# Optimization experiments

Hardware: AMD Instinct MI355X
Metric: run time of the kernel (lower is better)

## Reference

```python
import jax, jax.numpy as jnp
import numpy as np

N = 100000
E = 1600000
IN_C = 64
HID = 64
HEADS = 8
HEAD_D = HID // HEADS  # 8
LAYERS = 12
OUT_C = 10
STEPS = 5
NEG_SLOPE = 0.2


def setup_inputs() -> dict:
    key = jax.random.key(0)
    ks = jax.random.split(key, 12)
    x = jax.random.normal(ks[0], (N, IN_C), dtype=jnp.float32)
    edge_index = jax.random.randint(ks[1], (2, E), 0, N, dtype=jnp.int64)
    s = 0.1
    return {
        "x": x,
        "edge_index": edge_index,
        # GAT params: HEADS independent single-head GATConv(in -> HEAD_D)
        "gat_W": jax.random.normal(ks[2], (HEADS, IN_C, HEAD_D), dtype=jnp.float32) * s,
        "gat_a_src": jax.random.normal(ks[3], (HEADS, HEAD_D), dtype=jnp.float32) * s,
        "gat_a_dst": jax.random.normal(ks[4], (HEADS, HEAD_D), dtype=jnp.float32) * s,
        "gat_b": jax.random.normal(ks[5], (HEADS, HEAD_D), dtype=jnp.float32) * s,
        # GCN params: LAYERS x GCNConv(HID -> HID)
        "gcn_W": jax.random.normal(ks[6], (LAYERS, HID, HID), dtype=jnp.float32) * s,
        "gcn_b": jax.random.normal(ks[7], (LAYERS, HID), dtype=jnp.float32) * s,
        # final linear
        "fc_W": jax.random.normal(ks[8], (HID, OUT_C), dtype=jnp.float32) * s,
        "fc_b": jax.random.normal(ks[9], (OUT_C,), dtype=jnp.float32) * s,
    }


def _random_walk(x, row, col):
    # sparse A (COO: row=edge_index[0], col=edge_index[1], vals=1) applied num_steps times
    for _ in range(STEPS):
        x = jax.ops.segment_sum(x[col], row, num_segments=N)
    return x


def _gat_all_heads(x, W, a_src, a_dst, b, src, dst):
    # add self loops
    loop = jnp.arange(N, dtype=src.dtype)
    s2 = jnp.concatenate([src, loop])
    d2 = jnp.concatenate([dst, loop])
    h = jnp.einsum('nf,hfd->nhd', x, W)                      # [N,H,D]
    al_s = jnp.einsum('nhd,hd->nh', h, a_src)                # [N,H]
    al_d = jnp.einsum('nhd,hd->nh', h, a_dst)
    e = jax.nn.leaky_relu(al_s[s2] + al_d[d2], NEG_SLOPE)    # [E+N,H]
    m = jax.ops.segment_max(e, d2, num_segments=N)           # per-target max (self loops -> every node has >=1 edge)
    p = jnp.exp(e - m[d2])
    denom = jax.ops.segment_sum(p, d2, num_segments=N)
    alpha = p / denom[d2]                                    # [E+N,H]
    out = jax.ops.segment_sum(alpha[:, :, None] * h[s2], d2, num_segments=N)  # [N,H,D]
    out = out + b[None, :, :]
    return out.reshape(N, HEADS * HEAD_D)                    # concat heads -> [N,HID]


def _gcn(x, W, b, src, dst):
    loop = jnp.arange(N, dtype=src.dtype)
    s2 = jnp.concatenate([src, loop])
    d2 = jnp.concatenate([dst, loop])
    deg = jax.ops.segment_sum(jnp.ones(s2.shape[0], x.dtype), d2, num_segments=N)
    dis = jnp.where(deg > 0, jax.lax.rsqrt(jnp.maximum(deg, 1.0)), 0.0)
    norm = dis[s2] * dis[d2]                                 # [E+N]
    h = x @ W                                                # [N,HID]
    out = jax.ops.segment_sum(norm[:, None] * h[s2], d2, num_segments=N)
    return out + b


def reference(x, edge_index, gat_W, gat_a_src, gat_a_dst, gat_b, gcn_W, gcn_b, fc_W, fc_b):
    row, col = edge_index[0], edge_index[1]
    # 1) random walk diffusion
    x = _random_walk(x, row, col)
    # 2) multi-head GAT (8 independent heads, concatenated)
    x = _gat_all_heads(x, gat_W, gat_a_src, gat_a_dst, gat_b, row, col)
    # 3) deep residual GCN (faithful to the original indexing quirks)
    initial_residual = x
    for i in range(LAYERS):
        x = _gcn(x, gcn_W[i], gcn_b[i], row, col)
        if i > 0:
            x = x + initial_residual
            initial_residual = x
        x = jax.nn.relu(x)
        if i < LAYERS - 1:
            # note: i-1 == -1 at i==0 -> last layer, as in the torch code
            x = x + _gcn(x, gcn_W[i - 1], gcn_b[i - 1], row, col)
    # 4) final linear
    return x @ fc_W + fc_b
```

## Files before the change

kernel.cpp:

```cpp
#include <hip/hip_runtime.h>


typedef unsigned int u32;

#define BSH 7
#define RNGB 128
#define GEB 256

__device__ __forceinline__ float lrelu(float v) { return v > 0.f ? v : 0.2f * v; }
__device__ __forceinline__ float bf_lo(u32 w) { return __uint_as_float(w << 16); }
__device__ __forceinline__ float bf_hi(u32 w) { return __uint_as_float(w & 0xffff0000u); }
__device__ __forceinline__ u32 pack_bf16(float a, float b) {
  u32 ua = __float_as_uint(a); ua = ua + 0x7fffu + ((ua >> 16) & 1u);
  u32 ub = __float_as_uint(b); ub = ub + 0x7fffu + ((ub >> 16) & 1u);
  return (ua >> 16) | (ub & 0xffff0000u);
}
__device__ __forceinline__ void acc8(float* acc, uint4 q) {
  acc[0] += bf_lo(q.x); acc[1] += bf_hi(q.x);
  acc[2] += bf_lo(q.y); acc[3] += bf_hi(q.y);
  acc[4] += bf_lo(q.z); acc[5] += bf_hi(q.z);
  acc[6] += bf_lo(q.w); acc[7] += bf_hi(q.w);
}
__device__ __forceinline__ void fma8(float* acc, float p, uint4 q) {
  acc[0] = fmaf(p, bf_lo(q.x), acc[0]); acc[1] = fmaf(p, bf_hi(q.x), acc[1]);
  acc[2] = fmaf(p, bf_lo(q.y), acc[2]); acc[3] = fmaf(p, bf_hi(q.y), acc[3]);
  acc[4] = fmaf(p, bf_lo(q.z), acc[4]); acc[5] = fmaf(p, bf_hi(q.z), acc[5]);
  acc[6] = fmaf(p, bf_lo(q.w), acc[6]); acc[7] = fmaf(p, bf_hi(q.w), acc[7]);
}


__global__ __launch_bounds__(256) void k_hist(
    const int* __restrict__ ei, int E, int NB, int chunk,
    int* __restrict__ gHistA, int* __restrict__ gHistB) {
  __shared__ int hA[1024], hB[1024];
  for (int i = threadIdx.x; i < NB; i += 256) { hA[i] = 0; hB[i] = 0; }
  __syncthreads();
  int e0 = blockIdx.x * chunk;
  int e1 = min(E, e0 + chunk);
  for (int e = e0 + threadIdx.x; e < e1; e += 256) {
    int s = ei[e], d = ei[E + e];
    atomicAdd(&hA[s >> BSH], 1);
    atomicAdd(&hB[d >> BSH], 1);
  }
  __syncthreads();
  for (int i = threadIdx.x; i < NB; i += 256) {
    gHistA[blockIdx.x * NB + i] = hA[i];
    gHistB[blockIdx.x * NB + i] = hB[i];
  }
}

__global__ __launch_bounds__(256) void k_colscan(
    int* __restrict__ gHist, int* __restrict__ tot, int NB) {
  __shared__ int s[GEB];
  int b = blockIdx.x;
  int t = threadIdx.x;
  int v = gHist[t * NB + b];
  s[t] = v;
  __syncthreads();
  for (int d = 1; d < GEB; d <<= 1) {
    int u = (t >= d) ? s[t - d] : 0;
    __syncthreads();
    s[t] += u;
    __syncthreads();
  }
  gHist[t * NB + b] = s[t] - v;
  if (t == GEB - 1) tot[b] = s[t];
}

__global__ __launch_bounds__(1024) void k_bscan(
    const int* __restrict__ totA, const int* __restrict__ totB,
    int* __restrict__ baseA, int* __restrict__ baseB,
    int* __restrict__ offA, int* __restrict__ offB, int NB, int N, int E) {
  __shared__ int sa[1024], sb[1024];
  int t = threadIdx.x;
  int va = (t < NB) ? totA[t] : 0;
  int vb = (t < NB) ? totB[t] : 0;
  sa[t] = va; sb[t] = vb;
  __syncthreads();
  for (int d = 1; d < 1024; d <<= 1) {
    int ua = (t >= d) ? sa[t - d] : 0;
    int ub = (t >= d) ? sb[t - d] : 0;
    __syncthreads();
    sa[t] += ua; sb[t] += ub;
    __syncthreads();
  }
  if (t < NB) { baseA[t] = sa[t] - va; baseB[t] = sb[t] - vb; }
  if (t == 0) { offA[N] = E; offB[N] = E; }
}

__global__ __launch_bounds__(256) void k_scatter(
    const int* __restrict__ ei, int E, int NB, int chunk,
    const int* __restrict__ gHistA, const int* __restrict__ gHistB,
    const int* __restrict__ baseA, const int* __restrict__ baseB,
    int2* __restrict__ pairsA, int2* __restrict__ pairsB) {
  __shared__ int cA[1024], cB[1024];
  int g = blockIdx.x;
  for (int i = threadIdx.x; i < NB; i += 256) {
    cA[i] = baseA[i] + gHistA[g * NB + i];
    cB[i] = baseB[i] + gHistB[g * NB + i];
  }
  __syncthreads();
  int e0 = g * chunk;
  int e1 = min(E, e0 + chunk);
  for (int e = e0 + threadIdx.x; e < e1; e += 256) {
    int s = ei[e], d = ei[E + e];
    int pa = atomicAdd(&cA[s >> BSH], 1);
    pairsA[pa] = {s, d};
    int pb = atomicAdd(&cB[d >> BSH], 1);
    pairsB[pb] = {s, d};
  }
}

template <int KEY>
__global__ __launch_bounds__(256) void k_bucket(
    const int2* __restrict__ pairs, const int* __restrict__ base,
    const int* __restrict__ tot, int* __restrict__ off,
    int* __restrict__ idx, float* __restrict__ dis, int N) {
  __shared__ int cnt[RNGB], pfx[RNGB];
  int b = blockIdx.x;
  int node0 = b << BSH;
  int rng = min(RNGB, N - node0);
  int bstart = base[b], bcount = tot[b];
  for (int i = threadIdx.x; i < rng; i += 256) cnt[i] = 0;
  __syncthreads();
  for (int i = threadIdx.x; i < bcount; i += 256) {
    int2 p = pairs[bstart + i];
    int loc = (KEY == 0 ? p.x : p.y) - node0;
    atomicAdd(&cnt[loc], 1);
  }
  __syncthreads();
  if (threadIdx.x == 0) {
    int run = 0;
    for (int i = 0; i < rng; ++i) { pfx[i] = run; run += cnt[i]; }
  }
  __syncthreads();
  for (int i = threadIdx.x; i < rng; i += 256) {
    off[node0 + i] = bstart + pfx[i];
    if (KEY == 1) dis[node0 + i] = rsqrtf((float)(cnt[i] + 1));
  }
  __syncthreads();
  for (int i = threadIdx.x; i < bcount; i += 256) {
    int2 p = pairs[bstart + i];
    int loc = (KEY == 0 ? p.x : p.y) - node0;
    int pos = bstart + atomicAdd(&pfx[loc], 1);
    idx[pos] = (KEY == 0 ? p.y : p.x);
  }
}


template <int FIRST>
__global__ __launch_bounds__(256) void k_rw(
    const int* __restrict__ off, const int* __restrict__ idx,
    const float* __restrict__ Hf, const u32* __restrict__ Hb,
    u32* __restrict__ Xb, int n) {
  int lane = threadIdx.x & 63;
  int wid = threadIdx.x >> 6;
  int d0 = blockIdx.x * 8 + wid * 2;
  if (d0 >= n) return;
  int d1 = d0 + 1;
  bool has1 = d1 < n;
  int rg = lane >> 3, cg = lane & 7;
  const uint4* H4b = (const uint4*)Hb;
  const float4* H4f = (const float4*)Hf;
  int beg0 = off[d0], end0 = off[d0 + 1];
  int beg1 = has1 ? off[d1] : 0, end1 = has1 ? off[d1 + 1] : 0;
  int cnt0 = end0 - beg0, cnt1 = end1 - beg1;
  int cmax = cnt0 > cnt1 ? cnt0 : cnt1;
  float acc0[8], acc1[8];
#pragma unroll
  for (int i = 0; i < 8; ++i) { acc0[i] = 0.f; acc1[i] = 0.f; }
  for (int base = 0; base < cmax; base += 64) {
    int c0 = cnt0 - base; if (c0 > 64) c0 = 64;
    int c1 = cnt1 - base; if (c1 > 64) c1 = 64;
    int sidx0 = (lane < c0) ? idx[beg0 + base + lane] : -1;
    int sidx1 = (lane < c1) ? idx[beg1 + base + lane] : -1;
    int hi = c0 > c1 ? c0 : c1;
    int nI = (hi + 7) >> 3;
    int j = 0;
    for (; j + 2 <= nI; j += 2) {
      int s00 = __shfl(sidx0, j * 8 + rg, 64);
      int s01 = __shfl(sidx0, j * 8 + 8 + rg, 64);
      int s10 = __shfl(sidx1, j * 8 + rg, 64);
      int s11 = __shfl(sidx1, j * 8 + 8 + rg, 64);
      size_t a00 = (size_t)(s00 >= 0 ? s00 : 0);
      size_t a01 = (size_t)(s01 >= 0 ? s01 : 0);
      size_t a10 = (size_t)(s10 >= 0 ? s10 : 0);
      size_t a11 = (size_t)(s11 >= 0 ? s11 : 0);
      if (FIRST) {
        float4 x00 = H4f[a00 * 16 + cg * 2], y00 = H4f[a00 * 16 + cg * 2 + 1];
        float4 x01 = H4f[a01 * 16 + cg * 2], y01 = H4f[a01 * 16 + cg * 2 + 1];
        float4 x10 = H4f[a10 * 16 + cg * 2], y10 = H4f[a10 * 16 + cg * 2 + 1];
        float4 x11 = H4f[a11 * 16 + cg * 2], y11 = H4f[a11 * 16 + cg * 2 + 1];
        if (s00 < 0) { x00 = {0,0,0,0}; y00 = {0,0,0,0}; }
        if (s01 < 0) { x01 = {0,0,0,0}; y01 = {0,0,0,0}; }
        if (s10 < 0) { x10 = {0,0,0,0}; y10 = {0,0,0,0}; }
        if (s11 < 0) { x11 = {0,0,0,0}; y11 = {0,0,0,0}; }
        acc0[0] += x00.x; acc0[1] += x00.y; acc0[2] += x00.z; acc0[3] += x00.w;
        acc0[4] += y00.x; acc0[5] += y00.y; acc0[6] += y00.z; acc0[7] += y00.w;
        acc0[0] += x01.x; acc0[1] += x01.y; acc0[2] += x01.z; acc0[3] += x01.w;
        acc0[4] += y01.x; acc0[5] += y01.y; acc0[6] += y01.z; acc0[7] += y01.w;
        acc1[0] += x10.x; acc1[1] += x10.y; acc1[2] += x10.z; acc1[3] += x10.w;
        acc1[4] += y10.x; acc1[5] += y10.y; acc1[6] += y10.z; acc1[7] += y10.w;
        acc1[0] += x11.x; acc1[1] += x11.y; acc1[2] += x11.z; acc1[3] += x11.w;
        acc1[4] += y11.x; acc1[5] += y11.y; acc1[6] += y11.z; acc1[7] += y11.w;
      } else {
        uint4 q00 = H4b[a00 * 8 + cg];
        uint4 q01 = H4b[a01 * 8 + cg];
        uint4 q10 = H4b[a10 * 8 + cg];
        uint4 q11 = H4b[a11 * 8 + cg];
        if (s00 < 0) q00 = {0u,0u,0u,0u};
        if (s01 < 0) q01 = {0u,0u,0u,0u};
        if (s10 < 0) q10 = {0u,0u,0u,0u};
        if (s11 < 0) q11 = {0u,0u,0u,0u};
        acc8(acc0, q00);
        acc8(acc0, q01);
        acc8(acc1, q10);
        acc8(acc1, q11);
      }
    }
    if (j < nI) {
      int s00 = __shfl(sidx0, j * 8 + rg, 64);
      int s10 = __shfl(sidx1, j * 8 + rg, 64);
      size_t a00 = (size_t)(s00 >= 0 ? s00 : 0);
      size_t a10 = (size_t)(s10 >= 0 ? s10 : 0);
      if (FIRST) {
        float4 x00 = H4f[a00 * 16 + cg * 2], y00 = H4f[a00 * 16 + cg * 2 + 1];
        float4 x10 = H4f[a10 * 16 + cg * 2], y10 = H4f[a10 * 16 + cg * 2 + 1];
        if (s00 < 0) { x00 = {0,0,0,0}; y00 = {0,0,0,0}; }
        if (s10 < 0) { x10 = {0,0,0,0}; y10 = {0,0,0,0}; }
        acc0[0] += x00.x; acc0[1] += x00.y; acc0[2] += x00.z; acc0[3] += x00.w;
        acc0[4] += y00.x; acc0[5] += y00.y; acc0[6] += y00.z; acc0[7] += y00.w;
        acc1[0] += x10.x; acc1[1] += x10.y; acc1[2] += x10.z; acc1[3] += x10.w;
        acc1[4] += y10.x; acc1[5] += y10.y; acc1[6] += y10.z; acc1[7] += y10.w;
      } else {
        uint4 q00 = H4b[a00 * 8 + cg];
        uint4 q10 = H4b[a10 * 8 + cg];
        if (s00 < 0) q00 = {0u,0u,0u,0u};
        if (s10 < 0) q10 = {0u,0u,0u,0u};
        acc8(acc0, q00);
        acc8(acc1, q10);
      }
    }
  }
#pragma unroll
  for (int m = 8; m < 64; m <<= 1)
#pragma unroll
    for (int i = 0; i < 8; ++i) {
      acc0[i] += __shfl_xor(acc0[i], m, 64);
      acc1[i] += __shfl_xor(acc1[i], m, 64);
    }
  if (rg != 0) return;
  uint4 o0 = {pack_bf16(acc0[0], acc0[1]), pack_bf16(acc0[2], acc0[3]),
              pack_bf16(acc0[4], acc0[5]), pack_bf16(acc0[6], acc0[7])};
  ((uint4*)Xb)[(size_t)d0 * 8 + cg] = o0;
  if (has1) {
    uint4 o1 = {pack_bf16(acc1[0], acc1[1]), pack_bf16(acc1[2], acc1[3]),
                pack_bf16(acc1[4], acc1[5]), pack_bf16(acc1[6], acc1[7])};
    ((uint4*)Xb)[(size_t)d1 * 8 + cg] = o1;
  }
}


__global__ __launch_bounds__(256) void k_gat_gemm(
    const u32* __restrict__ Xb, const float* __restrict__ W,
    const float* __restrict__ asrc, const float* __restrict__ adst,
    u32* __restrict__ Hgb, float* __restrict__ al, int n) {
  __shared__ float Xs[64 * 65];
  int row0 = blockIdx.x * 64;
  for (int t = threadIdx.x; t < 512; t += 256) {
    int r = t >> 3, k8 = t & 7;
    int row = row0 + r;
    uint4 xw = (row < n) ? ((const uint4*)Xb)[(size_t)row * 8 + k8]
                         : uint4{0u, 0u, 0u, 0u};
    float* dst = &Xs[r * 65 + k8 * 8];
    dst[0] = bf_lo(xw.x); dst[1] = bf_hi(xw.x);
    dst[2] = bf_lo(xw.y); dst[3] = bf_hi(xw.y);
    dst[4] = bf_lo(xw.z); dst[5] = bf_hi(xw.z);
    dst[6] = bf_lo(xw.w); dst[7] = bf_hi(xw.w);
  }
  __syncthreads();
  int lane = threadIdx.x & 63;
  int w = __builtin_amdgcn_readfirstlane(threadIdx.x >> 6);
  int c0 = w * 16;
  int row = row0 + lane;
  float acc[16];
#pragma unroll
  for (int c = 0; c < 16; ++c) acc[c] = 0.f;
#pragma unroll 4
  for (int k = 0; k < 64; ++k) {
    float xk = Xs[lane * 65 + k];
#pragma unroll
    for (int c = 0; c < 16; ++c) {
      int gc = c0 + c;
      acc[c] = fmaf(xk, W[(gc >> 3) * 512 + k * 8 + (gc & 7)], acc[c]);
    }
  }
  if (row >= n) return;
  float s1a = 0.f, s2a = 0.f, s1b = 0.f, s2b = 0.f;
#pragma unroll
  for (int cc = 0; cc < 8; ++cc) {
    s1a = fmaf(acc[cc], asrc[c0 + cc], s1a);
    s2a = fmaf(acc[cc], adst[c0 + cc], s2a);
    s1b = fmaf(acc[8 + cc], asrc[c0 + 8 + cc], s1b);
    s2b = fmaf(acc[8 + cc], adst[c0 + 8 + cc], s2b);
  }
  float2* al2 = (float2*)al;
  al2[(size_t)row * 8 + w] = {s1a, s1b};
  al2[(size_t)row * 8 + 4 + w] = {s2a, s2b};
  uint4* H4 = (uint4*)Hgb;
  uint4 o0 = {pack_bf16(acc[0], acc[1]), pack_bf16(acc[2], acc[3]),
              pack_bf16(acc[4], acc[5]), pack_bf16(acc[6], acc[7])};
  uint4 o1 = {pack_bf16(acc[8], acc[9]), pack_bf16(acc[10], acc[11]),
              pack_bf16(acc[12], acc[13]), pack_bf16(acc[14], acc[15])};
  H4[(size_t)row * 8 + w * 2] = o0;
  H4[(size_t)row * 8 + w * 2 + 1] = o1;
}

__global__ __launch_bounds__(256) void k_gat_agg(
    const int* __restrict__ off, const int* __restrict__ idx,
    const u32* __restrict__ Hgb, const float* __restrict__ al,
    const float* __restrict__ bias, const float* __restrict__ dis,
    u32* __restrict__ Tout, float* __restrict__ R, int n) {
  int lane = threadIdx.x & 63;
  int wid = threadIdx.x >> 6;
  int d0 = blockIdx.x * 8 + wid * 2;
  if (d0 >= n) return;
  int d1 = d0 + 1;
  bool has1 = d1 < n;
  int rg = lane >> 3, cg = lane & 7;
  const uint4* H4b = (const uint4*)Hgb;
  float ald0 = al[(size_t)d0 * 16 + 8 + cg];
  float es0 = lrelu(al[(size_t)d0 * 16 + cg] + ald0);
  float ald1 = has1 ? al[(size_t)d1 * 16 + 8 + cg] : 0.f;
  float es1 = has1 ? lrelu(al[(size_t)d1 * 16 + cg] + ald1) : 0.f;
  int beg0 = off[d0], end0 = off[d0 + 1];
  int beg1 = has1 ? off[d1] : 0, end1 = has1 ? off[d1 + 1] : 0;
  int cnt0 = end0 - beg0, cnt1 = end1 - beg1;
  int cmax = cnt0 > cnt1 ? cnt0 : cnt1;
  float m0 = es0, m1 = es1;
  for (int base = 0; base < cmax; base += 64) {
    int c0 = cnt0 - base; if (c0 > 64) c0 = 64;
    int c1 = cnt1 - base; if (c1 > 64) c1 = 64;
    int sidx0 = (lane < c0) ? idx[beg0 + base + lane] : -1;
    int sidx1 = (lane < c1) ? idx[beg1 + base + lane] : -1;
    int hi = c0 > c1 ? c0 : c1;
    int nI = (hi + 7) >> 3;
    int j = 0;
    for (; j + 2 <= nI; j += 2) {
      int s00 = __shfl(sidx0, j * 8 + rg, 64);
      int s01 = __shfl(sidx0, j * 8 + 8 + rg, 64);
      int s10 = __shfl(sidx1, j * 8 + rg, 64);
      int s11 = __shfl(sidx1, j * 8 + 8 + rg, 64);
      float a00 = al[(size_t)(s00 >= 0 ? s00 : 0) * 16 + cg];
      float a01 = al[(size_t)(s01 >= 0 ? s01 : 0) * 16 + cg];
      float a10 = al[(size_t)(s10 >= 0 ? s10 : 0) * 16 + cg];
      float a11 = al[(size_t)(s11 >= 0 ? s11 : 0) * 16 + cg];
      if (s00 >= 0) m0 = fmaxf(m0, lrelu(a00 + ald0));
      if (s01 >= 0) m0 = fmaxf(m0, lrelu(a01 + ald0));
      if (s10 >= 0) m1 = fmaxf(m1, lrelu(a10 + ald1));
      if (s11 >= 0) m1 = fmaxf(m1, lrelu(a11 + ald1));
    }
    if (j < nI) {
      int s00 = __shfl(sidx0, j * 8 + rg, 64);
      int s10 = __shfl(sidx1, j * 8 + rg, 64);
      float a00 = al[(size_t)(s00 >= 0 ? s00 : 0) * 16 + cg];
      float a10 = al[(size_t)(s10 >= 0 ? s10 : 0) * 16 + cg];
      if (s00 >= 0) m0 = fmaxf(m0, lrelu(a00 + ald0));
      if (s10 >= 0) m1 = fmaxf(m1, lrelu(a10 + ald1));
    }
  }
#pragma unroll
  for (int mm = 8; mm < 64; mm <<= 1) {
    m0 = fmaxf(m0, __shfl_xor(m0, mm, 64));
    m1 = fmaxf(m1, __shfl_xor(m1, mm, 64));
  }
  float den0 = 0.f, den1 = 0.f;
  float acc0[8], acc1[8];
#pragma unroll
  for (int i = 0; i < 8; ++i) { acc0[i] = 0.f; acc1[i] = 0.f; }
  for (int base = 0; base < cmax; base += 64) {
    int c0 = cnt0 - base; if (c0 > 64) c0 = 64;
    int c1 = cnt1 - base; if (c1 > 64) c1 = 64;
    int sidx0 = (lane < c0) ? idx[beg0 + base + lane] : -1;
    int sidx1 = (lane < c1) ? idx[beg1 + base + lane] : -1;
    int hi = c0 > c1 ? c0 : c1;
    int nI = (hi + 7) >> 3;
    int j = 0;
    for (; j + 2 <= nI; j += 2) {
      int s00 = __shfl(sidx0, j * 8 + rg, 64);
      int s01 = __shfl(sidx0, j * 8 + 8 + rg, 64);
      int s10 = __shfl(sidx1, j * 8 + rg, 64);
      int s11 = __shfl(sidx1, j * 8 + 8 + rg, 64);
      size_t a00 = (size_t)(s00 >= 0 ? s00 : 0);
      size_t a01 = (size_t)(s01 >= 0 ? s01 : 0);
      size_t a10 = (size_t)(s10 >= 0 ? s10 : 0);
      size_t a11 = (size_t)(s11 >= 0 ? s11 : 0);
      float l00 = al[a00 * 16 + cg];
      float l01 = al[a01 * 16 + cg];
      float l10 = al[a10 * 16 + cg];
      float l11 = al[a11 * 16 + cg];
      uint4 q00 = H4b[a00 * 8 + cg];
      uint4 q01 = H4b[a01 * 8 + cg];
      uint4 q10 = H4b[a10 * 8 + cg];
      uint4 q11 = H4b[a11 * 8 + cg];
      float p00 = (s00 >= 0) ? __expf(lrelu(l00 + ald0) - m0) : 0.f;
      float p01 = (s01 >= 0) ? __expf(lrelu(l01 + ald0) - m0) : 0.f;
      float p10 = (s10 >= 0) ? __expf(lrelu(l10 + ald1) - m1) : 0.f;
      float p11 = (s11 >= 0) ? __expf(lrelu(l11 + ald1) - m1) : 0.f;
      den0 += p00; fma8(acc0, p00, q00);
      den0 += p01; fma8(acc0, p01, q01);
      den1 += p10; fma8(acc1, p10, q10);
      den1 += p11; fma8(acc1, p11, q11);
    }
    if (j < nI) {
      int s00 = __shfl(sidx0, j * 8 + rg, 64);
      int s10 = __shfl(sidx1, j * 8 + rg, 64);
      size_t a00 = (size_t)(s00 >= 0 ? s00 : 0);
      size_t a10 = (size_t)(s10 >= 0 ? s10 : 0);
      float l00 = al[a00 * 16 + cg];
      float l10 = al[a10 * 16 + cg];
      uint4 q00 = H4b[a00 * 8 + cg];
      uint4 q10 = H4b[a10 * 8 + cg];
      float p00 = (s00 >= 0) ? __expf(lrelu(l00 + ald0) - m0) : 0.f;
      float p10 = (s10 >= 0) ? __expf(lrelu(l10 + ald1) - m1) : 0.f;
      den0 += p00; fma8(acc0, p00, q00);
      den1 += p10; fma8(acc1, p10, q10);
    }
  }
#pragma unroll
  for (int mm = 8; mm < 64; mm <<= 1) {
#pragma unroll
    for (int i = 0; i < 8; ++i) {
      acc0[i] += __shfl_xor(acc0[i], mm, 64);
      acc1[i] += __shfl_xor(acc1[i], mm, 64);
    }
    den0 += __shfl_xor(den0, mm, 64);
    den1 += __shfl_xor(den1, mm, 64);
  }
  if (rg != 0) return;
#pragma unroll
  for (int nd = 0; nd < 2; ++nd) {
    if (nd == 1 && !has1) break;
    int d = nd == 0 ? d0 : d1;
    float* acc = nd == 0 ? acc0 : acc1;
    float es = nd == 0 ? es0 : es1;
    float m = nd == 0 ? m0 : m1;
    float den = nd == 0 ? den0 : den1;
    float pself = __expf(es - m);
    uint4 hw = H4b[(size_t)d * 8 + cg];
    float hs[8] = {bf_lo(hw.x), bf_hi(hw.x), bf_lo(hw.y), bf_hi(hw.y),
                   bf_lo(hw.z), bf_hi(hw.z), bf_lo(hw.w), bf_hi(hw.w)};
#pragma unroll
    for (int i = 0; i < 8; ++i) acc[i] = fmaf(pself, hs[i], acc[i]);
    den += pself;
    float inv = 1.f / den;
    float4 b0 = ((const float4*)bias)[cg * 2];
    float4 b1 = ((const float4*)bias)[cg * 2 + 1];
    float bv[8] = {b0.x, b0.y, b0.z, b0.w, b1.x, b1.y, b1.z, b1.w};
    float v[8];
#pragma unroll
    for (int i = 0; i < 8; ++i) v[i] = acc[i] * inv + bv[i];
    size_t o0 = (size_t)d * 16 + cg * 2;
    ((float4*)R)[o0] = {v[0], v[1], v[2], v[3]};
    ((float4*)R)[o0 + 1] = {v[4], v[5], v[6], v[7]};
    float dd = dis[d];
    uint4 tw = {pack_bf16(dd * v[0], dd * v[1]), pack_bf16(dd * v[2], dd * v[3]),
                pack_bf16(dd * v[4], dd * v[5]), pack_bf16(dd * v[6], dd * v[7])};
    ((uint4*)Tout)[(size_t)d * 8 + cg] = tw;
  }
}


enum { CG0 = 0, CGR = 1, CGRL = 2, CGD = 3 };

template <int MODE>
__global__ __launch_bounds__(256) void k_conv(
    const int* __restrict__ off, const int* __restrict__ idx,
    const u32* __restrict__ Tin, u32* __restrict__ Tout,
    const float* __restrict__ dis, const float* __restrict__ W,
    const float* __restrict__ bias, float* __restrict__ R,
    float* __restrict__ X, int n) {
  __shared__ float zs[4][128];
  int lane = threadIdx.x & 63;
  int wid = threadIdx.x >> 6;
  int d0 = blockIdx.x * 8 + wid * 2;
  if (d0 >= n) return;
  int d1 = d0 + 1;
  bool has1 = d1 < n;
  int rg = lane >> 3, cg = lane & 7;
  const uint4* T4 = (const uint4*)Tin;
  int beg0 = off[d0], end0 = off[d0 + 1];
  int beg1 = has1 ? off[d1] : 0, end1 = has1 ? off[d1 + 1] : 0;
  int cnt0 = end0 - beg0, cnt1 = end1 - beg1;
  int cmax = cnt0 > cnt1 ? cnt0 : cnt1;
  float acc0[8], acc1[8];
#pragma unroll
  for (int i = 0; i < 8; ++i) { acc0[i] = 0.f; acc1[i] = 0.f; }
  for (int base = 0; base < cmax; base += 64) {
    int c0 = cnt0 - base; if (c0 > 64) c0 = 64;
    int c1 = cnt1 - base; if (c1 > 64) c1 = 64;
    int sidx0 = (lane < c0) ? idx[beg0 + base + lane] : -1;
    int sidx1 = (lane < c1) ? idx[beg1 + base + lane] : -1;
    int hi = c0 > c1 ? c0 : c1;
    int nI = (hi + 7) >> 3;
    int j = 0;
    for (; j + 2 <= nI; j += 2) {
      int s00 = __shfl(sidx0, j * 8 + rg, 64);
      int s01 = __shfl(sidx0, j * 8 + 8 + rg, 64);
      int s10 = __shfl(sidx1, j * 8 + rg, 64);
      int s11 = __shfl(sidx1, j * 8 + 8 + rg, 64);
      size_t a00 = (size_t)(s00 >= 0 ? s00 : 0);
      size_t a01 = (size_t)(s01 >= 0 ? s01 : 0);
      size_t a10 = (size_t)(s10 >= 0 ? s10 : 0);
      size_t a11 = (size_t)(s11 >= 0 ? s11 : 0);
      uint4 q00 = T4[a00 * 8 + cg];
      uint4 q01 = T4[a01 * 8 + cg];
      uint4 q10 = T4[a10 * 8 + cg];
      uint4 q11 = T4[a11 * 8 + cg];
      if (s00 < 0) q00 = {0u,0u,0u,0u};
      if (s01 < 0) q01 = {0u,0u,0u,0u};
      if (s10 < 0) q10 = {0u,0u,0u,0u};
      if (s11 < 0) q11 = {0u,0u,0u,0u};
      acc8(acc0, q00);
      acc8(acc0, q01);
      acc8(acc1, q10);
      acc8(acc1, q11);
    }
    if (j < nI) {
      int s00 = __shfl(sidx0, j * 8 + rg, 64);
      int s10 = __shfl(sidx1, j * 8 + rg, 64);
      size_t a00 = (size_t)(s00 >= 0 ? s00 : 0);
      size_t a10 = (size_t)(s10 >= 0 ? s10 : 0);
      uint4 q00 = T4[a00 * 8 + cg];
      uint4 q10 = T4[a10 * 8 + cg];
      if (s00 < 0) q00 = {0u,0u,0u,0u};
      if (s10 < 0) q10 = {0u,0u,0u,0u};
      acc8(acc0, q00);
      acc8(acc1, q10);
    }
  }
#pragma unroll
  for (int m = 8; m < 64; m <<= 1)
#pragma unroll
    for (int i = 0; i < 8; ++i) {
      acc0[i] += __shfl_xor(acc0[i], m, 64);
      acc1[i] += __shfl_xor(acc1[i], m, 64);
    }
  float dd0 = dis[d0];
  uint4 ts0 = T4[(size_t)d0 * 8 + cg];
  float z0[8] = {dd0 * (acc0[0] + bf_lo(ts0.x)), dd0 * (acc0[1] + bf_hi(ts0.x)),
                 dd0 * (acc0[2] + bf_lo(ts0.y)), dd0 * (acc0[3] + bf_hi(ts0.y)),
                 dd0 * (acc0[4] + bf_lo(ts0.z)), dd0 * (acc0[5] + bf_hi(ts0.z)),
                 dd0 * (acc0[6] + bf_lo(ts0.w)), dd0 * (acc0[7] + bf_hi(ts0.w))};
  float dd1 = has1 ? dis[d1] : 0.f;
  uint4 ts1 = T4[(size_t)(has1 ? d1 : d0) * 8 + cg];
  float z1[8] = {dd1 * (acc1[0] + bf_lo(ts1.x)), dd1 * (acc1[1] + bf_hi(ts1.x)),
                 dd1 * (acc1[2] + bf_lo(ts1.y)), dd1 * (acc1[3] + bf_hi(ts1.y)),
                 dd1 * (acc1[4] + bf_lo(ts1.z)), dd1 * (acc1[5] + bf_hi(ts1.z)),
                 dd1 * (acc1[6] + bf_lo(ts1.w)), dd1 * (acc1[7] + bf_hi(ts1.w))};
  if (rg == 0) {
    float4* zp = (float4*)&zs[wid][cg * 8];
    zp[0] = {z0[0], z0[1], z0[2], z0[3]};
    zp[1] = {z0[4], z0[5], z0[6], z0[7]};
    float4* zq = (float4*)&zs[wid][64 + cg * 8];
    zq[0] = {z1[0], z1[1], z1[2], z1[3]};
    zq[1] = {z1[4], z1[5], z1[6], z1[7]};
  }
  asm volatile("s_waitcnt lgkmcnt(0)" ::: "memory");
  float outc0 = bias[lane];
  float outc1 = outc0;
  const float4* za = (const float4*)&zs[wid][0];
  const float4* zb = (const float4*)&zs[wid][64];
#pragma unroll 4
  for (int k4 = 0; k4 < 16; ++k4) {
    float4 a = za[k4];
    float4 b = zb[k4];
    int k = k4 * 4;
    float w0 = W[(k + 0) * 64 + lane];
    float w1 = W[(k + 1) * 64 + lane];
    float w2 = W[(k + 2) * 64 + lane];
    float w3 = W[(k + 3) * 64 + lane];
    outc0 = fmaf(a.x, w0, outc0); outc1 = fmaf(b.x, w0, outc1);
    outc0 = fmaf(a.y, w1, outc0); outc1 = fmaf(b.y, w1, outc1);
    outc0 = fmaf(a.z, w2, outc0); outc1 = fmaf(b.z, w2, outc1);
    outc0 = fmaf(a.w, w3, outc0); outc1 = fmaf(b.w, w3, outc1);
  }
#pragma unroll
  for (int nd = 0; nd < 2; ++nd) {
    if (nd == 1 && !has1) break;
    int d = nd == 0 ? d0 : d1;
    float outv = nd == 0 ? outc0 : outc1;
    size_t o = (size_t)d * 64 + lane;
    float res;
    if (MODE == CGD) {
      res = X[o] + outv;
    } else if (MODE == CG0) {
      res = fmaxf(outv, 0.f);
      X[o] = res;
    } else {
      float val = outv + R[o];
      R[o] = val;
      res = fmaxf(val, 0.f);
      X[o] = res;
    }
    if (MODE != CGRL) {
      float t = dis[d] * res;
      float tp = __shfl_xor(t, 1, 64);
      if (!(lane & 1))
        Tout[(size_t)d * 32 + (lane >> 1)] = pack_bf16(t, tp);
    }
  }
}


__global__ __launch_bounds__(256) void k_fc(
    const float* __restrict__ X, const float* __restrict__ W,
    const float* __restrict__ b, float* __restrict__ out, int n) {
  __shared__ float Wl[640];
  __shared__ float bl[10];
  for (int i = threadIdx.x; i < 640; i += 256) Wl[i] = W[i];
  if (threadIdx.x < 10) bl[threadIdx.x] = b[threadIdx.x];
  __syncthreads();
  int r = blockIdx.x * blockDim.x + threadIdx.x;
  if (r >= n) return;
  float acc[10];
#pragma unroll
  for (int c = 0; c < 10; ++c) acc[c] = bl[c];
#pragma unroll
  for (int k = 0; k < 64; ++k) {
    float xv = X[(size_t)r * 64 + k];
#pragma unroll
    for (int c = 0; c < 10; ++c) acc[c] = fmaf(xv, Wl[k * 10 + c], acc[c]);
  }
#pragma unroll
  for (int c = 0; c < 10; ++c) out[(size_t)r * 10 + c] = acc[c];
}


extern "C" void kernel_launch(void* const* d_in, const int* in_sizes, int n_in,
                              void* d_out, int out_size, void* d_ws, size_t ws_size,
                              hipStream_t stream) {
  const float* x_in  = (const float*)d_in[0];
  const int*   ei    = (const int*)d_in[1];
  const float* gatW  = (const float*)d_in[2];
  const float* gatAs = (const float*)d_in[3];
  const float* gatAd = (const float*)d_in[4];
  const float* gatB  = (const float*)d_in[5];
  const float* gcnW  = (const float*)d_in[6];
  const float* gcnB  = (const float*)d_in[7];
  const float* fcW   = (const float*)d_in[8];
  const float* fcB   = (const float*)d_in[9];
  float* out = (float*)d_out;

  const int N = in_sizes[0] / 64;
  const int E = in_sizes[1] / 2;
  const int NB = (N + RNGB - 1) >> BSH;
  const int chunk = (E + GEB - 1) / GEB;

  char* ws = (char*)d_ws;
  size_t o = 0;
  auto alloc = [&](size_t bytes) -> char* {
    char* p = ws + o;
    o = (o + bytes + 255) & ~(size_t)255;
    return p;
  };
  int* offA    = (int*)alloc((size_t)(N + 1) * 4);
  int* offB    = (int*)alloc((size_t)(N + 1) * 4);
  float* dis   = (float*)alloc((size_t)N * 4);
  int* idxA    = (int*)alloc((size_t)E * 4);
  int* idxB    = (int*)alloc((size_t)E * 4);
  int2* pairsA = (int2*)alloc((size_t)E * 8);
  int2* pairsB = (int2*)alloc((size_t)E * 8);
  int* gHistA  = (int*)alloc((size_t)GEB * NB * 4);
  int* gHistB  = (int*)alloc((size_t)GEB * NB * 4);
  int* totA    = (int*)alloc((size_t)NB * 4);
  int* totB    = (int*)alloc((size_t)NB * 4);
  int* baseA   = (int*)alloc((size_t)NB * 4);
  int* baseB   = (int*)alloc((size_t)NB * 4);
  float* al    = (float*)alloc((size_t)N * 16 * 4);
  u32* B0      = (u32*)alloc((size_t)N * 32 * 4);
  u32* B1      = (u32*)alloc((size_t)N * 32 * 4);
  float* X     = (float*)alloc((size_t)N * 64 * 4);
  float* R     = (float*)alloc((size_t)N * 64 * 4);

  int nbN = (N + 255) / 256;
  int nbAgg = (N + 7) / 8;
  int nbG = (N + 63) / 64;

  k_hist<<<GEB, 256, 0, stream>>>(ei, E, NB, chunk, gHistA, gHistB);
  k_colscan<<<NB, GEB, 0, stream>>>(gHistA, totA, NB);
  k_colscan<<<NB, GEB, 0, stream>>>(gHistB, totB, NB);
  k_bscan<<<1, 1024, 0, stream>>>(totA, totB, baseA, baseB, offA, offB, NB, N, E);
  k_scatter<<<GEB, 256, 0, stream>>>(ei, E, NB, chunk, gHistA, gHistB,
                                     baseA, baseB, pairsA, pairsB);
  k_bucket<0><<<NB, 256, 0, stream>>>(pairsA, baseA, totA, offA, idxA, nullptr, N);
  k_bucket<1><<<NB, 256, 0, stream>>>(pairsB, baseB, totB, offB, idxB, dis, N);

  k_rw<1><<<nbAgg, 256, 0, stream>>>(offA, idxA, x_in, nullptr, B0, N);
  k_rw<0><<<nbAgg, 256, 0, stream>>>(offA, idxA, nullptr, B0, B1, N);
  k_rw<0><<<nbAgg, 256, 0, stream>>>(offA, idxA, nullptr, B1, B0, N);
  k_rw<0><<<nbAgg, 256, 0, stream>>>(offA, idxA, nullptr, B0, B1, N);
  k_rw<0><<<nbAgg, 256, 0, stream>>>(offA, idxA, nullptr, B1, B0, N);

  k_gat_gemm<<<nbG, 256, 0, stream>>>(B0, gatW, gatAs, gatAd, B1, al, N);
  k_gat_agg<<<nbAgg, 256, 0, stream>>>(offB, idxB, B1, al, gatB, dis, B0, R, N);

  u32* Tc = B0;
  u32* Ta = B1;
  for (int i = 0; i < 12; ++i) {
    if (i == 0)
      k_conv<CG0><<<nbAgg, 256, 0, stream>>>(offB, idxB, Tc, Ta, dis,
                                             gcnW, gcnB, nullptr, X, N);
    else if (i == 11)
      k_conv<CGRL><<<nbAgg, 256, 0, stream>>>(offB, idxB, Tc, nullptr, dis,
                                              gcnW + i * 4096, gcnB + i * 64, R, X, N);
    else
      k_conv<CGR><<<nbAgg, 256, 0, stream>>>(offB, idxB, Tc, Ta, dis,
                                             gcnW + i * 4096, gcnB + i * 64, R, X, N);
    { u32* t = Tc; Tc = Ta; Ta = t; }
    if (i < 11) {
      int j = (i == 0) ? 11 : i - 1;
      k_conv<CGD><<<nbAgg, 256, 0, stream>>>(offB, idxB, Tc, Ta, dis,
                                             gcnW + j * 4096, gcnB + j * 64, nullptr, X, N);
      u32* t = Tc; Tc = Ta; Ta = t;
    }
  }

  k_fc<<<nbN, 256, 0, stream>>>(X, fcW, fcB, out, N);
}
```

Baseline: 1.895 ms.

## Tile GCN conv to 64 nodes per block with LDS-staged dense transform

Each k_conv block now aggregates 64 nodes (16 per wave, in pairs) into a padded 64x65 shared tile, then performs the 64x64 weight multiply with each lane owning one row and 16 output columns, using wave-uniform weight reads. Output writes become vectorized float4/uint4 stores per row. The aim is to amortize weight loads and make the dense transform compute-efficient rather than one output column per lane. The cost is a block-wide sync, more LDS per block (which may lower occupancy), and serialized per-wave gather loops over 8 node pairs.

```diff
diff --git a/kernel.cpp b/kernel.cpp
--- a/kernel.cpp
+++ b/kernel.cpp
@@ -480,135 +480,152 @@
     const float* __restrict__ dis, const float* __restrict__ W,
     const float* __restrict__ bias, float* __restrict__ R,
     float* __restrict__ X, int n) {
-  __shared__ float zs[4][128];
+  __shared__ float zs[64 * 65];
   int lane = threadIdx.x & 63;
   int wid = threadIdx.x >> 6;
-  int d0 = blockIdx.x * 8 + wid * 2;
-  if (d0 >= n) return;
-  int d1 = d0 + 1;
-  bool has1 = d1 < n;
   int rg = lane >> 3, cg = lane & 7;
+  int node0 = blockIdx.x * 64;
   const uint4* T4 = (const uint4*)Tin;
-  int beg0 = off[d0], end0 = off[d0 + 1];
-  int beg1 = has1 ? off[d1] : 0, end1 = has1 ? off[d1 + 1] : 0;
-  int cnt0 = end0 - beg0, cnt1 = end1 - beg1;
-  int cmax = cnt0 > cnt1 ? cnt0 : cnt1;
-  float acc0[8], acc1[8];
-#pragma unroll
-  for (int i = 0; i < 8; ++i) { acc0[i] = 0.f; acc1[i] = 0.f; }
-  for (int base = 0; base < cmax; base += 64) {
-    int c0 = cnt0 - base; if (c0 > 64) c0 = 64;
-    int c1 = cnt1 - base; if (c1 > 64) c1 = 64;
-    int sidx0 = (lane < c0) ? idx[beg0 + base + lane] : -1;
-    int sidx1 = (lane < c1) ? idx[beg1 + base + lane] : -1;
-    int hi = c0 > c1 ? c0 : c1;
-    int nI = (hi + 7) >> 3;
-    int j = 0;
-    for (; j + 2 <= nI; j += 2) {
-      int s00 = __shfl(sidx0, j * 8 + rg, 64);
-      int s01 = __shfl(sidx0, j * 8 + 8 + rg, 64);
-      int s10 = __shfl(sidx1, j * 8 + rg, 64);
-      int s11 = __shfl(sidx1, j * 8 + 8 + rg, 64);
-      size_t a00 = (size_t)(s00 >= 0 ? s00 : 0);
-      size_t a01 = (size_t)(s01 >= 0 ? s01 : 0);
-      size_t a10 = (size_t)(s10 >= 0 ? s10 : 0);
-      size_t a11 = (size_t)(s11 >= 0 ? s11 : 0);
-      uint4 q00 = T4[a00 * 8 + cg];
-      uint4 q01 = T4[a01 * 8 + cg];
-      uint4 q10 = T4[a10 * 8 + cg];
-      uint4 q11 = T4[a11 * 8 + cg];
-      if (s00 < 0) q00 = {0u,0u,0u,0u};
-      if (s01 < 0) q01 = {0u,0u,0u,0u};
-      if (s10 < 0) q10 = {0u,0u,0u,0u};
-      if (s11 < 0) q11 = {0u,0u,0u,0u};
-      acc8(acc0, q00);
-      acc8(acc0, q01);
-      acc8(acc1, q10);
-      acc8(acc1, q11);
-    }
-    if (j < nI) {
-      int s00 = __shfl(sidx0, j * 8 + rg, 64);
-      int s10 = __shfl(sidx1, j * 8 + rg, 64);
-      size_t a00 = (size_t)(s00 >= 0 ? s00 : 0);
-      size_t a10 = (size_t)(s10 >= 0 ? s10 : 0);
-      uint4 q00 = T4[a00 * 8 + cg];
-      uint4 q10 = T4[a10 * 8 + cg];
-      if (s00 < 0) q00 = {0u,0u,0u,0u};
-      if (s10 < 0) q10 = {0u,0u,0u,0u};
-      acc8(acc0, q00);
-      acc8(acc1, q10);
-    }
-  }
-#pragma unroll
-  for (int m = 8; m < 64; m <<= 1)
-#pragma unroll
-    for (int i = 0; i < 8; ++i) {
-      acc0[i] += __shfl_xor(acc0[i], m, 64);
-      acc1[i] += __shfl_xor(acc1[i], m, 64);
-    }
-  float dd0 = dis[d0];
-  uint4 ts0 = T4[(size_t)d0 * 8 + cg];
-  float z0[8] = {dd0 * (acc0[0] + bf_lo(ts0.x)), dd0 * (acc0[1] + bf_hi(ts0.x)),
-                 dd0 * (acc0[2] + bf_lo(ts0.y)), dd0 * (acc0[3] + bf_hi(ts0.y)),
-                 dd0 * (acc0[4] + bf_lo(ts0.z)), dd0 * (acc0[5] + bf_hi(ts0.z)),
-                 dd0 * (acc0[6] + bf_lo(ts0.w)), dd0 * (acc0[7] + bf_hi(ts0.w))};
-  float dd1 = has1 ? dis[d1] : 0.f;
-  uint4 ts1 = T4[(size_t)(has1 ? d1 : d0) * 8 + cg];
-  float z1[8] = {dd1 * (acc1[0] + bf_lo(ts1.x)), dd1 * (acc1[1] + bf_hi(ts1.x)),
-                 dd1 * (acc1[2] + bf_lo(ts1.y)), dd1 * (acc1[3] + bf_hi(ts1.y)),
-                 dd1 * (acc1[4] + bf_lo(ts1.z)), dd1 * (acc1[5] + bf_hi(ts1.z)),
-                 dd1 * (acc1[6] + bf_lo(ts1.w)), dd1 * (acc1[7] + bf_hi(ts1.w))};
-  if (rg == 0) {
-    float4* zp = (float4*)&zs[wid][cg * 8];
-    zp[0] = {z0[0], z0[1], z0[2], z0[3]};
-    zp[1] = {z0[4], z0[5], z0[6], z0[7]};
-    float4* zq = (float4*)&zs[wid][64 + cg * 8];
-    zq[0] = {z1[0], z1[1], z1[2], z1[3]};
-    zq[1] = {z1[4], z1[5], z1[6], z1[7]};
-  }
-  asm volatile("s_waitcnt lgkmcnt(0)" ::: "memory");
-  float outc0 = bias[lane];
-  float outc1 = outc0;
-  const float4* za = (const float4*)&zs[wid][0];
-  const float4* zb = (const float4*)&zs[wid][64];
+
+  for (int nd = 0; nd < 16; nd += 2) {
+    int ni = wid * 16 + nd;
+    int d0 = node0 + ni;
+    int d1 = d0 + 1;
+    bool has0 = d0 < n, has1 = d1 < n;
+    int beg0 = has0 ? off[d0] : 0, end0 = has0 ? off[d0 + 1] : 0;
+    int beg1 = has1 ? off[d1] : 0, end1 = has1 ? off[d1 + 1] : 0;
+    int cnt0 = end0 - beg0, cnt1 = end1 - beg1;
+    int cmax = cnt0 > cnt1 ? cnt0 : cnt1;
+    float acc0[8], acc1[8];
+#pragma unroll
+    for (int i = 0; i < 8; ++i) { acc0[i] = 0.f; acc1[i] = 0.f; }
+    for (int base = 0; base < cmax; base += 64) {
+      int cA = cnt0 - base; if (cA > 64) cA = 64;
+      int cB = cnt1 - base; if (cB > 64) cB = 64;
+      int sidx0 = (lane < cA) ? idx[beg0 + base + lane] : -1;
+      int sidx1 = (lane < cB) ? idx[beg1 + base + lane] : -1;
+      int hi = cA > cB ? cA : cB;
+      int nI = (hi + 7) >> 3;
+      int j = 0;
+      for (; j + 2 <= nI; j += 2) {
+        int s00 = __shfl(sidx0, j * 8 + rg, 64);
+        int s01 = __shfl(sidx0, j * 8 + 8 + rg, 64);
+        int s10 = __shfl(sidx1, j * 8 + rg, 64);
+        int s11 = __shfl(sidx1, j * 8 + 8 + rg, 64);
+        size_t a00 = (size_t)(s00 >= 0 ? s00 : 0);
+        size_t a01 = (size_t)(s01 >= 0 ? s01 : 0);
+        size_t a10 = (size_t)(s10 >= 0 ? s10 : 0);
+        size_t a11 = (size_t)(s11 >= 0 ? s11 : 0);
+        uint4 q00 = T4[a00 * 8 + cg];
+        uint4 q01 = T4[a01 * 8 + cg];
+        uint4 q10 = T4[a10 * 8 + cg];
+        uint4 q11 = T4[a11 * 8 + cg];
+        if (s00 < 0) q00 = {0u,0u,0u,0u};
+        if (s01 < 0) q01 = {0u,0u,0u,0u};
+        if (s10 < 0) q10 = {0u,0u,0u,0u};
+        if (s11 < 0) q11 = {0u,0u,0u,0u};
+        acc8(acc0, q00);
+        acc8(acc0, q01);
+        acc8(acc1, q10);
+        acc8(acc1, q11);
+      }
+      if (j < nI) {
+        int s00 = __shfl(sidx0, j * 8 + rg, 64);
+        int s10 = __shfl(sidx1, j * 8 + rg, 64);
+        size_t a00 = (size_t)(s00 >= 0 ? s00 : 0);
+        size_t a10 = (size_t)(s10 >= 0 ? s10 : 0);
+        uint4 q00 = T4[a00 * 8 + cg];
+        uint4 q10 = T4[a10 * 8 + cg];
+        if (s00 < 0) q00 = {0u,0u,0u,0u};
+        if (s10 < 0) q10 = {0u,0u,0u,0u};
+        acc8(acc0, q00);
+        acc8(acc1, q10);
+      }
+    }
+#pragma unroll
+    for (int m = 8; m < 64; m <<= 1)
+#pragma unroll
+      for (int i = 0; i < 8; ++i) {
+        acc0[i] += __shfl_xor(acc0[i], m, 64);
+        acc1[i] += __shfl_xor(acc1[i], m, 64);
+      }
+    if (rg == 0) {
+      if (has0) {
+        float dd = dis[d0];
+        uint4 ts = T4[(size_t)d0 * 8 + cg];
+        float* zp = &zs[ni * 65 + cg * 8];
+        zp[0] = dd * (acc0[0] + bf_lo(ts.x)); zp[1] = dd * (acc0[1] + bf_hi(ts.x));
+        zp[2] = dd * (acc0[2] + bf_lo(ts.y)); zp[3] = dd * (acc0[3] + bf_hi(ts.y));
+        zp[4] = dd * (acc0[4] + bf_lo(ts.z)); zp[5] = dd * (acc0[5] + bf_hi(ts.z));
+        zp[6] = dd * (acc0[6] + bf_lo(ts.w)); zp[7] = dd * (acc0[7] + bf_hi(ts.w));
+      }
+      if (has1) {
+        float dd = dis[d1];
+        uint4 ts = T4[(size_t)d1 * 8 + cg];
+        float* zp = &zs[(ni + 1) * 65 + cg * 8];
+        zp[0] = dd * (acc1[0] + bf_lo(ts.x)); zp[1] = dd * (acc1[1] + bf_hi(ts.x));
+        zp[2] = dd * (acc1[2] + bf_lo(ts.y)); zp[3] = dd * (acc1[3] + bf_hi(ts.y));
+        zp[4] = dd * (acc1[4] + bf_lo(ts.z)); zp[5] = dd * (acc1[5] + bf_hi(ts.z));
+        zp[6] = dd * (acc1[6] + bf_lo(ts.w)); zp[7] = dd * (acc1[7] + bf_hi(ts.w));
+      }
+    }
+  }
+  __syncthreads();
+
+  int c0 = __builtin_amdgcn_readfirstlane(wid) * 16;
+  int row = node0 + lane;
+  float acc[16];
+#pragma unroll
+  for (int c = 0; c < 16; ++c) acc[c] = 0.f;
 #pragma unroll 4
-  for (int k4 = 0; k4 < 16; ++k4) {
-    float4 a = za[k4];
-    float4 b = zb[k4];
-    int k = k4 * 4;
-    float w0 = W[(k + 0) * 64 + lane];
-    float w1 = W[(k + 1) * 64 + lane];
-    float w2 = W[(k + 2) * 64 + lane];
-    float w3 = W[(k + 3) * 64 + lane];
-    outc0 = fmaf(a.x, w0, outc0); outc1 = fmaf(b.x, w0, outc1);
-    outc0 = fmaf(a.y, w1, outc0); outc1 = fmaf(b.y, w1, outc1);
-    outc0 = fmaf(a.z, w2, outc0); outc1 = fmaf(b.z, w2, outc1);
-    outc0 = fmaf(a.w, w3, outc0); outc1 = fmaf(b.w, w3, outc1);
-  }
-#pragma unroll
-  for (int nd = 0; nd < 2; ++nd) {
-    if (nd == 1 && !has1) break;
-    int d = nd == 0 ? d0 : d1;
-    float outv = nd == 0 ? outc0 : outc1;
-    size_t o = (size_t)d * 64 + lane;
-    float res;
-    if (MODE == CGD) {
-      res = X[o] + outv;
-    } else if (MODE == CG0) {
-      res = fmaxf(outv, 0.f);
-      X[o] = res;
-    } else {
-      float val = outv + R[o];
-      R[o] = val;
-      res = fmaxf(val, 0.f);
-      X[o] = res;
-    }
-    if (MODE != CGRL) {
-      float t = dis[d] * res;
-      float tp = __shfl_xor(t, 1, 64);
-      if (!(lane & 1))
-        Tout[(size_t)d * 32 + (lane >> 1)] = pack_bf16(t, tp);
-    }
+  for (int k = 0; k < 64; ++k) {
+    float zk = zs[lane * 65 + k];
+#pragma unroll
+    for (int c = 0; c < 16; ++c)
+      acc[c] = fmaf(zk, W[k * 64 + c0 + c], acc[c]);
+  }
+  if (row >= n) return;
+  float res[16];
+  size_t rb = (size_t)row * 16 + (c0 >> 2);
+  if (MODE == CGD) {
+#pragma unroll
+    for (int q = 0; q < 4; ++q) {
+      float4 xv = ((const float4*)X)[rb + q];
+      res[q * 4 + 0] = xv.x + acc[q * 4 + 0] + bias[c0 + q * 4 + 0];
+      res[q * 4 + 1] = xv.y + acc[q * 4 + 1] + bias[c0 + q * 4 + 1];
+      res[q * 4 + 2] = xv.z + acc[q * 4 + 2] + bias[c0 + q * 4 + 2];
+      res[q * 4 + 3] = xv.w + acc[q * 4 + 3] + bias[c0 + q * 4 + 3];
+    }
+  } else if (MODE == CG0) {
+#pragma unroll
+    for (int c = 0; c < 16; ++c) res[c] = fmaxf(acc[c] + bias[c0 + c], 0.f);
+#pragma unroll
+    for (int q = 0; q < 4; ++q)
+      ((float4*)X)[rb + q] = {res[q * 4], res[q * 4 + 1], res[q * 4 + 2], res[q * 4 + 3]};
+  } else {
+#pragma unroll
+    for (int q = 0; q < 4; ++q) {
+      float4 rv = ((const float4*)R)[rb + q];
+      float v0 = acc[q * 4 + 0] + bias[c0 + q * 4 + 0] + rv.x;
+      float v1 = acc[q * 4 + 1] + bias[c0 + q * 4 + 1] + rv.y;
+      float v2 = acc[q * 4 + 2] + bias[c0 + q * 4 + 2] + rv.z;
+      float v3 = acc[q * 4 + 3] + bias[c0 + q * 4 + 3] + rv.w;
+      if (MODE == CGR) ((float4*)R)[rb + q] = {v0, v1, v2, v3};
+      res[q * 4 + 0] = fmaxf(v0, 0.f);
+      res[q * 4 + 1] = fmaxf(v1, 0.f);
+      res[q * 4 + 2] = fmaxf(v2, 0.f);
+      res[q * 4 + 3] = fmaxf(v3, 0.f);
+      ((float4*)X)[rb + q] = {res[q * 4], res[q * 4 + 1], res[q * 4 + 2], res[q * 4 + 3]};
+    }
+  }
+  if (MODE != CGRL) {
+    float sc = dis[row];
+    uint4 t0 = {pack_bf16(sc * res[0], sc * res[1]), pack_bf16(sc * res[2], sc * res[3]),
+                pack_bf16(sc * res[4], sc * res[5]), pack_bf16(sc * res[6], sc * res[7])};
+    uint4 t1 = {pack_bf16(sc * res[8], sc * res[9]), pack_bf16(sc * res[10], sc * res[11]),
+                pack_bf16(sc * res[12], sc * res[13]), pack_bf16(sc * res[14], sc * res[15])};
+    ((uint4*)Tout)[(size_t)row * 8 + (c0 >> 3)] = t0;
+    ((uint4*)Tout)[(size_t)row * 8 + (c0 >> 3) + 1] = t1;
   }
 }
 
@@ -709,19 +726,19 @@
   u32* Ta = B1;
   for (int i = 0; i < 12; ++i) {
     if (i == 0)
-      k_conv<CG0><<<nbAgg, 256, 0, stream>>>(offB, idxB, Tc, Ta, dis,
-                                             gcnW, gcnB, nullptr, X, N);
+      k_conv<CG0><<<nbG, 256, 0, stream>>>(offB, idxB, Tc, Ta, dis,
+                                           gcnW, gcnB, nullptr, X, N);
     else if (i == 11)
-      k_conv<CGRL><<<nbAgg, 256, 0, stream>>>(offB, idxB, Tc, nullptr, dis,
-                                              gcnW + i * 4096, gcnB + i * 64, R, X, N);
+      k_conv<CGRL><<<nbG, 256, 0, stream>>>(offB, idxB, Tc, nullptr, dis,
+                                            gcnW + i * 4096, gcnB + i * 64, R, X, N);
     else
-      k_conv<CGR><<<nbAgg, 256, 0, stream>>>(offB, idxB, Tc, Ta, dis,
-                                             gcnW + i * 4096, gcnB + i * 64, R, X, N);
+      k_conv<CGR><<<nbG, 256, 0, stream>>>(offB, idxB, Tc, Ta, dis,
+                                           gcnW + i * 4096, gcnB + i * 64, R, X, N);
     { u32* t = Tc; Tc = Ta; Ta = t; }
     if (i < 11) {
       int j = (i == 0) ? 11 : i - 1;
-      k_conv<CGD><<<nbAgg, 256, 0, stream>>>(offB, idxB, Tc, Ta, dis,
-                                             gcnW + j * 4096, gcnB + j * 64, nullptr, X, N);
+      k_conv<CGD><<<nbG, 256, 0, stream>>>(offB, idxB, Tc, Ta, dis,
+                                           gcnW + j * 4096, gcnB + j * 64, nullptr, X, N);
       u32* t = Tc; Tc = Ta; Ta = t;
     }
   }
```

Result: no change. 1.862 ms (-1.8%).
